# Performance work log

Measured on AMD Instinct MI355X. Metric: run time of the kernel, lower is better.

The kernel has to match this reference:

```python
import jax, jax.numpy as jnp
import numpy as np

B, N, DIM, H, DH = 32, 1024, 512, 8, 64
SCALE = DH ** -0.5


def setup_inputs() -> dict:
    key = jax.random.key(0)
    k1, k2, k3, k4 = jax.random.split(key, 4)
    x = jax.random.normal(k1, (B, N, DIM), dtype=jnp.float32)
    W_qkv = jax.random.normal(k2, (DIM, 3 * H * DH), dtype=jnp.float32) * (DIM ** -0.5)
    W_out = jax.random.normal(k3, (H * DH, DIM), dtype=jnp.float32) * ((H * DH) ** -0.5)
    b_out = jnp.zeros((DIM,), dtype=jnp.float32)
    decay_mask = jax.random.uniform(k4, (1, H, N, N), dtype=jnp.float32)
    return {"x": x, "W_qkv": W_qkv, "W_out": W_out, "b_out": b_out,
            "decay_mask": decay_mask}


def reference(x, W_qkv, W_out, b_out, decay_mask):
    b, n, _ = x.shape
    qkv = x @ W_qkv                                  # [b, n, 3*h*d]
    q, k, v = jnp.split(qkv, 3, axis=-1)
    reshape = lambda t: t.reshape(b, n, H, DH).transpose(0, 2, 1, 3)  # b h n d
    q, k, v = reshape(q), reshape(k), reshape(v)
    dots = jnp.einsum('bhid,bhjd->bhij', q, k) * SCALE
    attn = jax.nn.softmax(dots, axis=-1)
    attn = attn * decay_mask                          # post-softmax decay mask
    out = jnp.einsum('bhij,bhjd->bhid', attn, v)      # [b, h, n, d]
    out = out.transpose(0, 2, 1, 3).reshape(b, n, H * DH)
    return out @ W_out + b_out
```

## Files before the change

### kernel.cpp

```cpp
#include <hip/hip_runtime.h>
#include <hip/hip_fp16.h>
#include <math.h>

#define Bb 32
#define Nn 1024
#define DIMc 512
#define Hh 8
#define DHd 64
#define GK 512

typedef __attribute__((ext_vector_type(8))) short short8;
typedef __attribute__((ext_vector_type(8))) _Float16 half8;
typedef __attribute__((ext_vector_type(2))) __fp16 fp16x2;
typedef __attribute__((ext_vector_type(4))) float floatx4;

#define MFMA16 __builtin_amdgcn_mfma_f32_16x16x32_f16

#if __has_builtin(__builtin_amdgcn_exp2f)
#define EXP2(x) __builtin_amdgcn_exp2f(x)
#else
#define EXP2(x) __expf((x) * 0.6931471805599453f)
#endif

__device__ __forceinline__ unsigned short f16_bits(float f) {
    return __half_as_ushort(__float2half(f));
}
__device__ __forceinline__ int cvt_pk_f16(float a, float b) {
    fp16x2 r = __builtin_amdgcn_cvt_pkrtz(a, b);
    return __builtin_bit_cast(int, r);
}

__global__ __launch_bounds__(256) void transpose_half_kernel(
    const float* __restrict__ src, int K, int N,
    unsigned short* __restrict__ dh)
{
    __shared__ float T[32][33];
    const int tid = threadIdx.x;
    const int c = tid & 31, r0 = tid >> 5;
    const int nb = blockIdx.x * 32, kb = blockIdx.y * 32;
    #pragma unroll
    for (int i = 0; i < 4; ++i)
        T[r0 + i * 8][c] = src[(size_t)(kb + r0 + i * 8) * N + nb + c];
    __syncthreads();
    #pragma unroll
    for (int i = 0; i < 4; ++i) {
        int n = r0 + i * 8;
        dh[(size_t)(nb + n) * K + kb + c] = f16_bits(T[c][n]);
    }
}

__global__ __launch_bounds__(256) void decay_to_half_kernel(
    const float* __restrict__ D, unsigned short* __restrict__ D16)
{
    size_t i = ((size_t)blockIdx.x * 256 + threadIdx.x) * 4;
    float4 v = *(const float4*)(D + i);
    ushort4 o;
    o.x = f16_bits(v.x * 0.00390625f);
    o.y = f16_bits(v.y * 0.00390625f);
    o.z = f16_bits(v.z * 0.00390625f);
    o.w = f16_bits(v.w * 0.00390625f);
    *(ushort4*)(D16 + i) = o;
}

__global__ __launch_bounds__(256) void x_to_half_kernel(
    const float* __restrict__ X, unsigned short* __restrict__ Xf)
{
    size_t i = ((size_t)blockIdx.x * 256 + threadIdx.x) * 8;
    float4 a = *(const float4*)(X + i);
    float4 b = *(const float4*)(X + i + 4);
    float f[8] = {a.x, a.y, a.z, a.w, b.x, b.y, b.z, b.w};
    short8 o;
    #pragma unroll
    for (int e = 0; e < 8; ++e) o[e] = (short)f16_bits(f[e]);
    *(short8*)(Xf + i) = o;
}

__device__ __forceinline__ void gload_lds16(const unsigned short* g, unsigned short* l) {
    __builtin_amdgcn_global_load_lds(
        (const __attribute__((address_space(1))) unsigned int*)g,
        (__attribute__((address_space(3))) unsigned int*)l,
        16, 0, 0);
}

__global__ __launch_bounds__(256) void gemm_qkv_mfma(
    const unsigned short* __restrict__ Xf, const unsigned short* __restrict__ Wf,
    unsigned short* __restrict__ Qf, unsigned short* __restrict__ Kf,
    unsigned short* __restrict__ Vt)
{
    __shared__ union {
        struct { unsigned short Af[2][4096], Bf[2][4096]; } s;
        unsigned short bounce[128][136];
    } u;

    const int tid  = threadIdx.x;
    const int w    = tid >> 6;
    const int lane = tid & 63;
    const int quad = lane >> 4;
    const int l16  = lane & 15;
    const int lb = blockIdx.x;
    const int wg = (lb & 7) * 384 + (lb >> 3);
    const int n0 = (wg % 12) * 128;
    const int m0 = (wg / 12) * 128;
    const int wm = w >> 1, wn = w & 1;

    floatx4 acc[4][4];
    #pragma unroll
    for (int im = 0; im < 4; ++im)
        #pragma unroll
        for (int in = 0; in < 4; ++in)
            acc[im][in] = (floatx4){0.f, 0.f, 0.f, 0.f};

    #pragma unroll
    for (int i = 0; i < 2; ++i) {
        const int row = i * 64 + w * 16 + l16;
        const size_t aoff = (size_t)(m0 + row) * GK + quad * 8;
        const size_t boff = (size_t)(n0 + row) * GK + quad * 8;
        const int lbe = (i * 4 + w) * 512;
        gload_lds16(Xf + aoff, &u.s.Af[0][lbe]);
        gload_lds16(Wf + boff, &u.s.Bf[0][lbe]);
    }

    int cur = 0;
    for (int k0 = 0; k0 < GK; k0 += 32) {
        __syncthreads();
        if (k0 + 32 < GK) {
            const int kn = k0 + 32;
            #pragma unroll
            for (int i = 0; i < 2; ++i) {
                const int row = i * 64 + w * 16 + l16;
                const size_t aoff = (size_t)(m0 + row) * GK + kn + quad * 8;
                const size_t boff = (size_t)(n0 + row) * GK + kn + quad * 8;
                const int lbe = (i * 4 + w) * 512;
                gload_lds16(Xf + aoff, &u.s.Af[cur ^ 1][lbe]);
                gload_lds16(Wf + boff, &u.s.Bf[cur ^ 1][lbe]);
            }
        }

        half8 faf[4], fbf[4];
        #pragma unroll
        for (int t = 0; t < 4; ++t) {
            const int ca = ((wm * 4 + t) * 4 + quad) * 16 + l16;
            faf[t] = *(const half8*)&u.s.Af[cur][ca * 8];
            const int cb = ((wn * 4 + t) * 4 + quad) * 16 + l16;
            fbf[t] = *(const half8*)&u.s.Bf[cur][cb * 8];
        }
        #pragma unroll
        for (int im = 0; im < 4; ++im)
            #pragma unroll
            for (int in = 0; in < 4; ++in)
                acc[im][in] = MFMA16(faf[im], fbf[in], acc[im][in], 0, 0, 0);
        cur ^= 1;
    }

    const int which = n0 >> 9;
    const int b    = m0 >> 10;
    const int tokb = m0 & 1023;
    if (which < 2) {
        unsigned short* OUT = which ? Kf : Qf;
        const float sc = which ? 1.0f : 0.18033688011112042f;
        #pragma unroll
        for (int im = 0; im < 4; ++im) {
            const int tok = tokb + wm * 64 + im * 16 + quad * 4;
            #pragma unroll
            for (int in = 0; in < 4; ++in) {
                const int ncol = n0 + wn * 64 + in * 16 + l16;
                const int h = (ncol & 511) >> 6, d = ncol & 63;
                const size_t base = ((size_t)(b * Hh + h) * Nn + tok) * DHd + d;
                #pragma unroll
                for (int r = 0; r < 4; ++r)
                    OUT[base + (size_t)r * DHd] = f16_bits(acc[im][in][r] * sc);
            }
        }
    } else {
        __syncthreads();
        #pragma unroll
        for (int im = 0; im < 4; ++im)
            #pragma unroll
            for (int in = 0; in < 4; ++in)
                #pragma unroll
                for (int r = 0; r < 4; ++r)
                    u.bounce[wm * 64 + im * 16 + quad * 4 + r][wn * 64 + in * 16 + l16] =
                        f16_bits(acc[im][in][r]);
        __syncthreads();
        const int c = tid >> 1, tq = (tid & 1) * 64;
        const int h = ((n0 + c) & 511) >> 6, d = c & 63;
        unsigned short* vbase = Vt + ((size_t)(b * Hh + h) * DHd + d) * Nn + tokb;
        #pragma unroll
        for (int uu = 0; uu < 8; ++uu) {
            short8 v8;
            #pragma unroll
            for (int e = 0; e < 8; ++e)
                v8[e] = (short)u.bounce[tq + uu * 8 + e][c];
            *(short8*)&vbase[tq + uu * 8] = v8;
        }
    }
}

__global__ __launch_bounds__(256) void attn_mfma_kernel(
    const unsigned short* __restrict__ Qf, const unsigned short* __restrict__ Kf,
    const unsigned short* __restrict__ Vt, const unsigned short* __restrict__ D16,
    unsigned short* __restrict__ AOf)
{
    __shared__ unsigned short Kfs[32][72];
    __shared__ unsigned short Vts[64][40];

    const int tid  = threadIdx.x;
    const int wave = tid >> 6;
    const int lane = tid & 63;
    const int quad = lane >> 4;
    const int l16  = lane & 15;
    const int lb   = blockIdx.x;
    const int xcd  = lb & 7;
    const int r_   = lb >> 3;
    const int h    = r_ >> 6;
    const int rem  = r_ & 63;
    const int i0   = (rem >> 2) << 6;
    const int b    = xcd * 4 + (rem & 3);
    const int bh   = b * 8 + h;
    const int iw   = i0 + wave * 16;

    const size_t qoff = ((size_t)bh * Nn + iw + l16) * DHd + quad * 8;
    const half8 qf0 = *(const half8*)(Qf + qoff);
    const half8 qf1 = *(const half8*)(Qf + qoff + 32);

    floatx4 o_acc[4];
    #pragma unroll
    for (int nt = 0; nt < 4; ++nt) o_acc[nt] = (floatx4){0.f, 0.f, 0.f, 0.f};
    float l = 0.f;

    const int sj  = tid >> 3, sc2 = (tid & 7) * 8;
    const int prow = ((sj >> 2) & 1) * 16 + ((sj >> 3) << 2) + (sj & 3);
    const int vd  = tid >> 2, vj8 = (tid & 3) * 8;
    const unsigned short* Dp = D16 + ((size_t)h * Nn + iw + l16) * Nn + quad * 8;

    const unsigned short* kpf = Kf + (size_t)bh * Nn * DHd + (size_t)sj * DHd + sc2;
    const unsigned short* vpv = Vt + (size_t)bh * DHd * Nn + (size_t)vd * Nn + vj8;

    short8 pk_f = *(const short8*)kpf; kpf += 32 * DHd;
    short8 pk_v = *(const short8*)vpv; vpv += 32;

    for (int j0 = 0; j0 < Nn; j0 += 32) {
        const short8 dc = *(const short8*)(Dp + j0);
        __syncthreads();
        *(short8*)&Kfs[prow][sc2] = pk_f;
        *(short8*)&Vts[vd][vj8]   = pk_v;
        __syncthreads();
        {
            pk_f = *(const short8*)kpf; kpf += 32 * DHd;
            pk_v = *(const short8*)vpv; vpv += 32;
        }

        floatx4 sacc[2];
        #pragma unroll
        for (int nh = 0; nh < 2; ++nh) {
            const int kr = nh * 16 + l16;
            half8 kf0 = *(const half8*)&Kfs[kr][quad * 8];
            half8 kf1 = *(const half8*)&Kfs[kr][32 + quad * 8];
            floatx4 a = (floatx4){0.f, 0.f, 0.f, 0.f};
            a = MFMA16(kf0, qf0, a, 0, 0, 0);
            a = MFMA16(kf1, qf1, a, 0, 0, 0);
            sacc[nh] = a;
        }

        float p[8];
        #pragma unroll
        for (int e = 0; e < 4; ++e) p[e]     = EXP2(sacc[0][e]);
        #pragma unroll
        for (int e = 0; e < 4; ++e) p[4 + e] = EXP2(sacc[1][e]);
        l += ((p[0] + p[1]) + (p[2] + p[3])) + ((p[4] + p[5]) + (p[6] + p[7]));

        union { int i4[4]; half8 v8; } pfu;
        const int* dci = (const int*)&dc;
        #pragma unroll
        for (int e = 0; e < 4; ++e) {
            fp16x2 pv = __builtin_bit_cast(fp16x2, cvt_pk_f16(p[2 * e], p[2 * e + 1]));
            fp16x2 dv = __builtin_bit_cast(fp16x2, dci[e]);
            pfu.i4[e] = __builtin_bit_cast(int, pv * dv);
        }
        #pragma unroll
        for (int nt = 0; nt < 4; ++nt) {
            half8 vf = *(const half8*)&Vts[nt * 16 + l16][quad * 8];
            o_acc[nt] = MFMA16(pfu.v8, vf, o_acc[nt], 0, 0, 0);
        }
    }

    float lsum = l;
    lsum += __shfl_xor(lsum, 16);
    lsum += __shfl_xor(lsum, 32);
    const float inv = 256.f / lsum;
    float ir[4];
    #pragma unroll
    for (int r = 0; r < 4; ++r) ir[r] = __shfl(inv, quad * 4 + r);
    const size_t aob = ((size_t)b * Nn + i0 + wave * 16) * DIMc + h * DHd;
    #pragma unroll
    for (int nt = 0; nt < 4; ++nt)
        #pragma unroll
        for (int r = 0; r < 4; ++r) {
            const size_t off = aob + (size_t)(quad * 4 + r) * DIMc + nt * 16 + l16;
            AOf[off] = f16_bits(o_acc[nt][r] * ir[r]);
        }
}

__global__ __launch_bounds__(256) void gemm_out_mfma(
    const unsigned short* __restrict__ Af, const unsigned short* __restrict__ Wf,
    const float* __restrict__ bias, float* __restrict__ C)
{
    __shared__ struct { unsigned short Aa[2][4096], Bf[2][4096]; } s;

    const int tid  = threadIdx.x;
    const int w    = tid >> 6;
    const int lane = tid & 63;
    const int quad = lane >> 4;
    const int l16  = lane & 15;
    const int lb = blockIdx.x;
    const int wg = (lb & 7) * 128 + (lb >> 3);
    const int n0 = (wg & 3) * 128;
    const int m0 = (wg >> 2) * 128;
    const int wm = w >> 1, wn = w & 1;

    floatx4 acc[4][4];
    #pragma unroll
    for (int im = 0; im < 4; ++im)
        #pragma unroll
        for (int in = 0; in < 4; ++in)
            acc[im][in] = (floatx4){0.f, 0.f, 0.f, 0.f};

    #pragma unroll
    for (int i = 0; i < 2; ++i) {
        const int row = i * 64 + w * 16 + l16;
        const size_t aoff = (size_t)(m0 + row) * GK + quad * 8;
        const size_t boff = (size_t)(n0 + row) * GK + quad * 8;
        const int lbe = (i * 4 + w) * 512;
        gload_lds16(Af + aoff, &s.Aa[0][lbe]);
        gload_lds16(Wf + boff, &s.Bf[0][lbe]);
    }

    int cur = 0;
    for (int k0 = 0; k0 < GK; k0 += 32) {
        __syncthreads();
        if (k0 + 32 < GK) {
            const int kn = k0 + 32;
            #pragma unroll
            for (int i = 0; i < 2; ++i) {
                const int row = i * 64 + w * 16 + l16;
                const size_t aoff = (size_t)(m0 + row) * GK + kn + quad * 8;
                const size_t boff = (size_t)(n0 + row) * GK + kn + quad * 8;
                const int lbe = (i * 4 + w) * 512;
                gload_lds16(Af + aoff, &s.Aa[cur ^ 1][lbe]);
                gload_lds16(Wf + boff, &s.Bf[cur ^ 1][lbe]);
            }
        }

        half8 faf[4], fbf[4];
        #pragma unroll
        for (int t = 0; t < 4; ++t) {
            const int ca = ((wm * 4 + t) * 4 + quad) * 16 + l16;
            faf[t] = *(const half8*)&s.Aa[cur][ca * 8];
            const int cb = ((wn * 4 + t) * 4 + quad) * 16 + l16;
            fbf[t] = *(const half8*)&s.Bf[cur][cb * 8];
        }
        #pragma unroll
        for (int im = 0; im < 4; ++im)
            #pragma unroll
            for (int in = 0; in < 4; ++in)
                acc[im][in] = MFMA16(faf[im], fbf[in], acc[im][in], 0, 0, 0);
        cur ^= 1;
    }

    float biasv[4];
    #pragma unroll
    for (int in = 0; in < 4; ++in) biasv[in] = bias[n0 + wn * 64 + in * 16 + l16];
    #pragma unroll
    for (int im = 0; im < 4; ++im)
        #pragma unroll
        for (int in = 0; in < 4; ++in) {
            const int mrow = m0 + wm * 64 + im * 16 + quad * 4;
            const int ncol = n0 + wn * 64 + in * 16 + l16;
            #pragma unroll
            for (int r = 0; r < 4; ++r)
                C[(size_t)(mrow + r) * DIMc + ncol] = acc[im][in][r] + biasv[in];
        }
}

extern "C" void kernel_launch(void* const* d_in, const int* in_sizes, int n_in,
                              void* d_out, int out_size, void* d_ws, size_t ws_size,
                              hipStream_t stream)
{
    const float* x     = (const float*)d_in[0];
    const float* Wqkv  = (const float*)d_in[1];
    const float* Wout  = (const float*)d_in[2];
    const float* bout  = (const float*)d_in[3];
    const float* decay = (const float*)d_in[4];

    const size_t E = (size_t)32768 * 512;
    unsigned short* p = (unsigned short*)d_ws;
    unsigned short* Qf  = p; p += E;
    unsigned short* Kf  = p; p += E;
    unsigned short* Vt  = p; p += E;
    unsigned short* AOf = p; p += E;
    unsigned short* Wq  = p; p += 786432;
    unsigned short* Wo  = p; p += 262144;
    unsigned short* D16 = p;
    unsigned short* Xf = AOf;

    transpose_half_kernel<<<dim3(48, 16), 256, 0, stream>>>(Wqkv, 512, 1536, Wq);
    transpose_half_kernel<<<dim3(16, 16), 256, 0, stream>>>(Wout, 512, 512, Wo);
    decay_to_half_kernel<<<dim3(8192), 256, 0, stream>>>(decay, D16);
    x_to_half_kernel<<<dim3(8192), 256, 0, stream>>>(x, Xf);
    gemm_qkv_mfma<<<dim3(3072), 256, 0, stream>>>(Xf, Wq, Qf, Kf, Vt);
    attn_mfma_kernel<<<dim3(4096), 256, 0, stream>>>(Qf, Kf, Vt, D16, AOf);
    gemm_out_mfma<<<dim3(1024), 256, 0, stream>>>(AOf, Wo, bout, (float*)d_out);
}
```

Measured before the change: 304.1 us.

## Process two query tiles per wave and double-buffer K/V in LDS

Measured after the change: 288.1 us. 1.06x faster.

```diff
diff --git a/kernel.cpp b/kernel.cpp
--- a/kernel.cpp
+++ b/kernel.cpp
@@ -201,8 +201,8 @@
     const unsigned short* __restrict__ Vt, const unsigned short* __restrict__ D16,
     unsigned short* __restrict__ AOf)
 {
-    __shared__ unsigned short Kfs[32][72];
-    __shared__ unsigned short Vts[64][40];
+    __shared__ unsigned short Kfs[2][32][72];
+    __shared__ unsigned short Vts[2][64][40];
 
     const int tid  = threadIdx.x;
     const int wave = tid >> 6;
@@ -212,92 +212,125 @@
     const int lb   = blockIdx.x;
     const int xcd  = lb & 7;
     const int r_   = lb >> 3;
-    const int h    = r_ >> 6;
-    const int rem  = r_ & 63;
-    const int i0   = (rem >> 2) << 6;
+    const int h    = r_ >> 5;
+    const int rem  = r_ & 31;
+    const int i0   = (rem >> 2) << 7;
     const int b    = xcd * 4 + (rem & 3);
     const int bh   = b * 8 + h;
-    const int iw   = i0 + wave * 16;
-
-    const size_t qoff = ((size_t)bh * Nn + iw + l16) * DHd + quad * 8;
-    const half8 qf0 = *(const half8*)(Qf + qoff);
-    const half8 qf1 = *(const half8*)(Qf + qoff + 32);
-
-    floatx4 o_acc[4];
-    #pragma unroll
-    for (int nt = 0; nt < 4; ++nt) o_acc[nt] = (floatx4){0.f, 0.f, 0.f, 0.f};
-    float l = 0.f;
+    const int iw   = i0 + wave * 32;
+
+    const size_t qoffA = ((size_t)bh * Nn + iw + l16) * DHd + quad * 8;
+    const size_t qoffB = qoffA + (size_t)16 * DHd;
+    const half8 qA0 = *(const half8*)(Qf + qoffA);
+    const half8 qA1 = *(const half8*)(Qf + qoffA + 32);
+    const half8 qB0 = *(const half8*)(Qf + qoffB);
+    const half8 qB1 = *(const half8*)(Qf + qoffB + 32);
+
+    floatx4 oA[4], oB[4];
+    #pragma unroll
+    for (int nt = 0; nt < 4; ++nt) {
+        oA[nt] = (floatx4){0.f, 0.f, 0.f, 0.f};
+        oB[nt] = (floatx4){0.f, 0.f, 0.f, 0.f};
+    }
+    float lA = 0.f, lB = 0.f;
 
     const int sj  = tid >> 3, sc2 = (tid & 7) * 8;
     const int prow = ((sj >> 2) & 1) * 16 + ((sj >> 3) << 2) + (sj & 3);
     const int vd  = tid >> 2, vj8 = (tid & 3) * 8;
-    const unsigned short* Dp = D16 + ((size_t)h * Nn + iw + l16) * Nn + quad * 8;
+    const unsigned short* DpA = D16 + ((size_t)h * Nn + iw + l16) * Nn + quad * 8;
+    const unsigned short* DpB = DpA + (size_t)16 * Nn;
 
     const unsigned short* kpf = Kf + (size_t)bh * Nn * DHd + (size_t)sj * DHd + sc2;
     const unsigned short* vpv = Vt + (size_t)bh * DHd * Nn + (size_t)vd * Nn + vj8;
 
     short8 pk_f = *(const short8*)kpf; kpf += 32 * DHd;
     short8 pk_v = *(const short8*)vpv; vpv += 32;
-
+    *(short8*)&Kfs[0][prow][sc2] = pk_f;
+    *(short8*)&Vts[0][vd][vj8]   = pk_v;
+    __syncthreads();
+
+    int cur = 0;
     for (int j0 = 0; j0 < Nn; j0 += 32) {
-        const short8 dc = *(const short8*)(Dp + j0);
-        __syncthreads();
-        *(short8*)&Kfs[prow][sc2] = pk_f;
-        *(short8*)&Vts[vd][vj8]   = pk_v;
-        __syncthreads();
-        {
-            pk_f = *(const short8*)kpf; kpf += 32 * DHd;
-            pk_v = *(const short8*)vpv; vpv += 32;
-        }
-
-        floatx4 sacc[2];
+        pk_f = *(const short8*)kpf; kpf += 32 * DHd;
+        pk_v = *(const short8*)vpv; vpv += 32;
+        const short8 dcA = *(const short8*)(DpA + j0);
+        const short8 dcB = *(const short8*)(DpB + j0);
+
+        floatx4 sA[2], sB[2];
         #pragma unroll
         for (int nh = 0; nh < 2; ++nh) {
             const int kr = nh * 16 + l16;
-            half8 kf0 = *(const half8*)&Kfs[kr][quad * 8];
-            half8 kf1 = *(const half8*)&Kfs[kr][32 + quad * 8];
+            half8 kf0 = *(const half8*)&Kfs[cur][kr][quad * 8];
+            half8 kf1 = *(const half8*)&Kfs[cur][kr][32 + quad * 8];
             floatx4 a = (floatx4){0.f, 0.f, 0.f, 0.f};
-            a = MFMA16(kf0, qf0, a, 0, 0, 0);
-            a = MFMA16(kf1, qf1, a, 0, 0, 0);
-            sacc[nh] = a;
-        }
-
-        float p[8];
-        #pragma unroll
-        for (int e = 0; e < 4; ++e) p[e]     = EXP2(sacc[0][e]);
-        #pragma unroll
-        for (int e = 0; e < 4; ++e) p[4 + e] = EXP2(sacc[1][e]);
-        l += ((p[0] + p[1]) + (p[2] + p[3])) + ((p[4] + p[5]) + (p[6] + p[7]));
-
-        union { int i4[4]; half8 v8; } pfu;
-        const int* dci = (const int*)&dc;
+            a = MFMA16(kf0, qA0, a, 0, 0, 0);
+            a = MFMA16(kf1, qA1, a, 0, 0, 0);
+            sA[nh] = a;
+            floatx4 c = (floatx4){0.f, 0.f, 0.f, 0.f};
+            c = MFMA16(kf0, qB0, c, 0, 0, 0);
+            c = MFMA16(kf1, qB1, c, 0, 0, 0);
+            sB[nh] = c;
+        }
+
+        float pA[8], pB[8];
         #pragma unroll
         for (int e = 0; e < 4; ++e) {
-            fp16x2 pv = __builtin_bit_cast(fp16x2, cvt_pk_f16(p[2 * e], p[2 * e + 1]));
-            fp16x2 dv = __builtin_bit_cast(fp16x2, dci[e]);
-            pfu.i4[e] = __builtin_bit_cast(int, pv * dv);
+            pA[e]     = EXP2(sA[0][e]);
+            pA[4 + e] = EXP2(sA[1][e]);
+            pB[e]     = EXP2(sB[0][e]);
+            pB[4 + e] = EXP2(sB[1][e]);
+        }
+        lA += ((pA[0] + pA[1]) + (pA[2] + pA[3])) + ((pA[4] + pA[5]) + (pA[6] + pA[7]));
+        lB += ((pB[0] + pB[1]) + (pB[2] + pB[3])) + ((pB[4] + pB[5]) + (pB[6] + pB[7]));
+
+        union { int i4[4]; half8 v8; } pfA, pfB;
+        const int* dA = (const int*)&dcA;
+        const int* dB = (const int*)&dcB;
+        #pragma unroll
+        for (int e = 0; e < 4; ++e) {
+            fp16x2 pa = __builtin_bit_cast(fp16x2, cvt_pk_f16(pA[2 * e], pA[2 * e + 1]));
+            fp16x2 da = __builtin_bit_cast(fp16x2, dA[e]);
+            pfA.i4[e] = __builtin_bit_cast(int, pa * da);
+            fp16x2 pb = __builtin_bit_cast(fp16x2, cvt_pk_f16(pB[2 * e], pB[2 * e + 1]));
+            fp16x2 db = __builtin_bit_cast(fp16x2, dB[e]);
+            pfB.i4[e] = __builtin_bit_cast(int, pb * db);
         }
         #pragma unroll
         for (int nt = 0; nt < 4; ++nt) {
-            half8 vf = *(const half8*)&Vts[nt * 16 + l16][quad * 8];
-            o_acc[nt] = MFMA16(pfu.v8, vf, o_acc[nt], 0, 0, 0);
-        }
-    }
-
-    float lsum = l;
-    lsum += __shfl_xor(lsum, 16);
-    lsum += __shfl_xor(lsum, 32);
-    const float inv = 256.f / lsum;
-    float ir[4];
-    #pragma unroll
-    for (int r = 0; r < 4; ++r) ir[r] = __shfl(inv, quad * 4 + r);
-    const size_t aob = ((size_t)b * Nn + i0 + wave * 16) * DIMc + h * DHd;
+            half8 vf = *(const half8*)&Vts[cur][nt * 16 + l16][quad * 8];
+            oA[nt] = MFMA16(pfA.v8, vf, oA[nt], 0, 0, 0);
+            oB[nt] = MFMA16(pfB.v8, vf, oB[nt], 0, 0, 0);
+        }
+
+        *(short8*)&Kfs[cur ^ 1][prow][sc2] = pk_f;
+        *(short8*)&Vts[cur ^ 1][vd][vj8]   = pk_v;
+        __syncthreads();
+        cur ^= 1;
+    }
+
+    float lsA = lA;
+    lsA += __shfl_xor(lsA, 16);
+    lsA += __shfl_xor(lsA, 32);
+    float lsB = lB;
+    lsB += __shfl_xor(lsB, 16);
+    lsB += __shfl_xor(lsB, 32);
+    const float invA = 256.f / lsA;
+    const float invB = 256.f / lsB;
+    float irA[4], irB[4];
+    #pragma unroll
+    for (int r = 0; r < 4; ++r) {
+        irA[r] = __shfl(invA, quad * 4 + r);
+        irB[r] = __shfl(invB, quad * 4 + r);
+    }
+    const size_t aobA = ((size_t)b * Nn + iw) * DIMc + h * DHd;
+    const size_t aobB = aobA + (size_t)16 * DIMc;
     #pragma unroll
     for (int nt = 0; nt < 4; ++nt)
         #pragma unroll
         for (int r = 0; r < 4; ++r) {
-            const size_t off = aob + (size_t)(quad * 4 + r) * DIMc + nt * 16 + l16;
-            AOf[off] = f16_bits(o_acc[nt][r] * ir[r]);
+            const size_t ro = (size_t)(quad * 4 + r) * DIMc + nt * 16 + l16;
+            AOf[aobA + ro] = f16_bits(oA[nt][r] * irA[r]);
+            AOf[aobB + ro] = f16_bits(oB[nt][r] * irB[r]);
         }
 }
 
@@ -408,6 +441,6 @@
     decay_to_half_kernel<<<dim3(8192), 256, 0, stream>>>(decay, D16);
     x_to_half_kernel<<<dim3(8192), 256, 0, stream>>>(x, Xf);
     gemm_qkv_mfma<<<dim3(3072), 256, 0, stream>>>(Xf, Wq, Qf, Kf, Vt);
-    attn_mfma_kernel<<<dim3(4096), 256, 0, stream>>>(Qf, Kf, Vt, D16, AOf);
+    attn_mfma_kernel<<<dim3(2048), 256, 0, stream>>>(Qf, Kf, Vt, D16, AOf);
     gemm_out_mfma<<<dim3(1024), 256, 0, stream>>>(AOf, Wo, bout, (float*)d_out);
 }
```
